# Performance work log

Measured on AMD Instinct MI355X. Metric: run time of the kernel, lower is better.

## Reference

```python
import jax, jax.numpy as jnp
import numpy as np

EPS = 1e-5

def _conv1x1(x, w, b=None):
    # x: (B, Cin, H, W), w: (Cout, Cin) -> (B, Cout, H, W)
    y = jnp.einsum('bchw,oc->bohw', x, w)
    if b is not None:
        y = y + b[None, :, None, None]
    return y

def setup_inputs() -> dict:
    key = jax.random.key(0)
    ks = jax.random.split(key, 14)
    B, C, I = 4, 256, 128
    Ha = Wa = 64
    Hd = Wd = 128
    s = 0.05
    return {
        'detect':  jax.random.normal(ks[0], (B, C, Hd, Wd), jnp.float32),
        'aim':     jax.random.normal(ks[1], (B, C, Ha, Wa), jnp.float32),
        'g_w':     jax.random.normal(ks[2], (I, C), jnp.float32) * s,
        'g_b':     jax.random.normal(ks[3], (I,), jnp.float32) * s,
        'theta_w': jax.random.normal(ks[4], (I, C), jnp.float32) * s,
        'theta_b': jax.random.normal(ks[5], (I,), jnp.float32) * s,
        'phi_w':   jax.random.normal(ks[6], (I, C), jnp.float32) * s,
        'phi_b':   jax.random.normal(ks[7], (I,), jnp.float32) * s,
        'q_w':     jax.random.normal(ks[8], (C, I), jnp.float32) * s,
        'q_b':     jax.random.normal(ks[9], (C,), jnp.float32) * s,
        'bn_gamma': jax.random.normal(ks[10], (C,), jnp.float32),
        'bn_beta':  jax.random.normal(ks[11], (C,), jnp.float32),
        'bn_mean':  jax.random.normal(ks[12], (C,), jnp.float32),
        'bn_var':   jax.random.uniform(ks[13], (C,), jnp.float32) + 0.5,
    }

def reference(detect, aim, g_w, g_b, theta_w, theta_b, phi_w, phi_b,
              q_w, q_b, bn_gamma, bn_beta, bn_mean, bn_var):
    B, C, Hd, Wd = detect.shape
    _, _, Ha, Wa = aim.shape
    Na = Ha * Wa
    Nd = Hd * Wd
    I = g_w.shape[0]

    # 1x1 conv projections, flattened to token sequences
    a_g   = _conv1x1(aim, g_w, g_b).reshape(B, I, Na)        # g(aim)
    th_a  = _conv1x1(aim, theta_w, theta_b).reshape(B, I, Na)
    ph_d  = _conv1x1(detect, phi_w, phi_b).reshape(B, I, Nd)
    # (d_x = g(detect) is dead code in the original forward; omitted)

    # f = theta_x @ phi_x : (B, Na, Nd); permuted -> (B, Nd, Na); N = Na
    f = jnp.einsum('bia,bid->bad', th_a, ph_d)               # (B, Na, Nd)
    inv_n = jnp.float32(1.0 / Na)
    # non_det = (f^T / Na) @ a_x : (B, Nd, I) -> permute -> (B, I, Nd)
    non = jnp.einsum('bad,bia->bid', f * inv_n, a_g)         # (B, I, Nd)
    non = non.reshape(B, I, Hd, Wd)

    # Q: 1x1 conv (I -> C) + BatchNorm (inference mode, running stats)
    y = _conv1x1(non, q_w, q_b)
    inv_std = jax.lax.rsqrt(bn_var + EPS)
    y = (y - bn_mean[None, :, None, None]) * (bn_gamma * inv_std)[None, :, None, None] \
        + bn_beta[None, :, None, None]

    return y + detect
```

## Files before the change

### kernel.cpp

```cpp
#include <hip/hip_runtime.h>

constexpr int BB   = 4;
constexpr int CCH  = 256;
constexpr int IDIM = 128;
constexpr int NAa  = 4096;
constexpr int NDd  = 16384;
constexpr int PAD  = 320;
constexpr float NAinv = 1.0f / 4096.0f;

typedef __bf16 bf16x8 __attribute__((ext_vector_type(8)));
typedef float  f32x4  __attribute__((ext_vector_type(4)));

__device__ inline unsigned short f2bfu(float f) {
    unsigned u = __float_as_uint(f);
    u += 0x7FFFu + ((u >> 16) & 1u);
    return (unsigned short)(u >> 16);
}

__global__ __launch_bounds__(256) void k_conv(const float* __restrict__ aim,
                                              unsigned short* __restrict__ Abf,
                                              float* __restrict__ r) {
    const int row = blockIdx.x;
    const float* src = aim + (long)row * NAa;
    unsigned short* dst = Abf + (long)row * NAa;
    const int t = threadIdx.x;
    float s = 0.f;
    #pragma unroll
    for (int j = 0; j < 4; ++j) {
        const int e = (j * 256 + t) * 4;
        float4 v = *(const float4*)(src + e);
        s += v.x + v.y + v.z + v.w;
        ushort4 o; o.x = f2bfu(v.x); o.y = f2bfu(v.y); o.z = f2bfu(v.z); o.w = f2bfu(v.w);
        *(ushort4*)(dst + e) = o;
    }
    __shared__ float red[256];
    red[t] = s; __syncthreads();
    for (int st = 128; st > 0; st >>= 1) { if (t < st) red[t] += red[t + st]; __syncthreads(); }
    if (t == 0) r[row] = red[0];
}

__global__ __launch_bounds__(256) void k_prep(const float* __restrict__ qw,
                                              const float* __restrict__ gw,
                                              const float* __restrict__ gb,
                                              const float* __restrict__ thw,
                                              const float* __restrict__ thb,
                                              const float* __restrict__ phw,
                                              const float* __restrict__ phb,
                                              unsigned short* __restrict__ Ph,
                                              unsigned short* __restrict__ Rt) {
    const int idx = blockIdx.x * 256 + threadIdx.x;
    if (idx < CCH * PAD) {
        const int o = idx / PAD, c = idx - o * PAD;
        float acc = 0.f;
        if (c <= 256) {
            for (int i = 0; i < IDIM; ++i)
                acc += qw[o * IDIM + i] * ((c < 256) ? gw[i * CCH + c] : gb[i]);
        }
        Ph[idx] = f2bfu(acc);
    } else {
        const int id2 = idx - CCH * PAD;
        const int c2 = id2 / PAD, k = id2 - c2 * PAD;
        float acc = 0.f;
        if (k <= 256 && c2 <= 256) {
            for (int i = 0; i < IDIM; ++i) {
                const float av = (k < 256) ? thw[i * CCH + k] : thb[i];
                const float bv = (c2 < 256) ? phw[i * CCH + c2] : phb[i];
                acc += av * bv;
            }
        }
        Rt[id2] = f2bfu(acc);
    }
}

__global__ __launch_bounds__(64) void k_S(const unsigned short* __restrict__ Abf,
                                          float* __restrict__ Spart) {
    const int z = blockIdx.z, b = z >> 3, chunk = z & 7;
    const unsigned short* A = Abf + (long)b * CCH * NAa;
    const int lane = threadIdx.x, quad = lane >> 4, l16 = lane & 15;
    const int mb = blockIdx.y * 64, nb = blockIdx.x * 64;
    const int kb = chunk * 512;
    f32x4 acc[4][4] = {};
    for (int ks = 0; ks < 16; ++ks) {
        const int k = kb + ks * 32 + quad * 8;
        bf16x8 af[4], bfr[4];
        #pragma unroll
        for (int i = 0; i < 4; ++i) af[i]  = *(const bf16x8*)(A + (long)(mb + i * 16 + l16) * NAa + k);
        #pragma unroll
        for (int j = 0; j < 4; ++j) bfr[j] = *(const bf16x8*)(A + (long)(nb + j * 16 + l16) * NAa + k);
        #pragma unroll
        for (int i = 0; i < 4; ++i)
            #pragma unroll
            for (int j = 0; j < 4; ++j)
                acc[i][j] = __builtin_amdgcn_mfma_f32_16x16x32_bf16(af[i], bfr[j], acc[i][j], 0, 0, 0);
    }
    float* o = Spart + (long)z * CCH * CCH;
    #pragma unroll
    for (int i = 0; i < 4; ++i)
        #pragma unroll
        for (int j = 0; j < 4; ++j)
            #pragma unroll
            for (int reg = 0; reg < 4; ++reg)
                o[(long)(mb + i * 16 + quad * 4 + reg) * CCH + nb + j * 16 + l16] = acc[i][j][reg];
}

__global__ __launch_bounds__(256) void k_red(const float* __restrict__ Spart,
                                             const float* __restrict__ r,
                                             unsigned short* __restrict__ Shat) {
    const int b = blockIdx.y;
    const int idx = blockIdx.x * 256 + threadIdx.x;
    const int k = idx / PAD, n = idx - k * PAD;
    float v = 0.f;
    if (k < 256 && n < 256) {
        #pragma unroll
        for (int p = 0; p < 8; ++p)
            v += Spart[(long)(b * 8 + p) * CCH * CCH + k * CCH + n];
    } else if (k == 256 && n < 256) v = r[b * CCH + n];
    else if (n == 256 && k < 256)   v = r[b * CCH + k];
    else if (k == 256 && n == 256)  v = 4096.0f;
    Shat[(long)b * PAD * PAD + idx] = f2bfu(v);
}

__global__ __launch_bounds__(64) void k_t1(const unsigned short* __restrict__ Ph,
                                           const unsigned short* __restrict__ Sh,
                                           unsigned short* __restrict__ Th) {
    const int b = blockIdx.z;
    const unsigned short* S = Sh + (long)b * PAD * PAD;
    unsigned short* T = Th + (long)b * CCH * PAD;
    const int n0 = blockIdx.x * 64, m0 = blockIdx.y * 64;
    const int lane = threadIdx.x, quad = lane >> 4, l16 = lane & 15;
    f32x4 acc[4][4] = {};
    for (int kt = 0; kt < PAD; kt += 32) {
        bf16x8 af[4], bfr[4];
        #pragma unroll
        for (int i = 0; i < 4; ++i) af[i]  = *(const bf16x8*)(Ph + (long)(m0 + i * 16 + l16) * PAD + kt + quad * 8);
        #pragma unroll
        for (int j = 0; j < 4; ++j) bfr[j] = *(const bf16x8*)(S  + (long)(n0 + j * 16 + l16) * PAD + kt + quad * 8);
        #pragma unroll
        for (int i = 0; i < 4; ++i)
            #pragma unroll
            for (int j = 0; j < 4; ++j)
                acc[i][j] = __builtin_amdgcn_mfma_f32_16x16x32_bf16(af[i], bfr[j], acc[i][j], 0, 0, 0);
    }
    #pragma unroll
    for (int i = 0; i < 4; ++i)
        #pragma unroll
        for (int j = 0; j < 4; ++j)
            #pragma unroll
            for (int reg = 0; reg < 4; ++reg)
                T[(long)(m0 + i * 16 + quad * 4 + reg) * PAD + n0 + j * 16 + l16] = f2bfu(acc[i][j][reg]);
}

__global__ __launch_bounds__(64) void k_t2(const unsigned short* __restrict__ Th,
                                           const unsigned short* __restrict__ Rt,
                                           const float* __restrict__ qb,
                                           const float* __restrict__ gamma,
                                           const float* __restrict__ beta,
                                           const float* __restrict__ mean,
                                           const float* __restrict__ var,
                                           unsigned short* __restrict__ W5u,
                                           float* __restrict__ b5) {
    const int b = blockIdx.z;
    const unsigned short* A = Th + (long)b * CCH * PAD;
    const int n0 = blockIdx.x * 64, m0 = blockIdx.y * 64;
    const int lane = threadIdx.x, quad = lane >> 4, l16 = lane & 15;
    f32x4 acc[4][4] = {};
    for (int kt = 0; kt < PAD; kt += 32) {
        bf16x8 af[4], bfr[4];
        #pragma unroll
        for (int i = 0; i < 4; ++i) af[i]  = *(const bf16x8*)(A  + (long)(m0 + i * 16 + l16) * PAD + kt + quad * 8);
        #pragma unroll
        for (int j = 0; j < 4; ++j) bfr[j] = *(const bf16x8*)(Rt + (long)(n0 + j * 16 + l16) * PAD + kt + quad * 8);
        #pragma unroll
        for (int i = 0; i < 4; ++i)
            #pragma unroll
            for (int j = 0; j < 4; ++j)
                acc[i][j] = __builtin_amdgcn_mfma_f32_16x16x32_bf16(af[i], bfr[j], acc[i][j], 0, 0, 0);
    }
    #pragma unroll
    for (int i = 0; i < 4; ++i) {
        #pragma unroll
        for (int reg = 0; reg < 4; ++reg) {
            const int o = m0 + i * 16 + quad * 4 + reg;
            const float s = gamma[o] * rsqrtf(var[o] + 1e-5f);
            #pragma unroll
            for (int j = 0; j < 4; ++j) {
                const int c2 = n0 + j * 16 + l16;
                const float val = acc[i][j][reg] * s * NAinv;
                if (c2 < CCH)
                    W5u[((long)b * CCH + o) * CCH + c2] = f2bfu(val + (o == c2 ? 1.0f : 0.0f));
                else if (c2 == CCH)
                    b5[b * CCH + o] = val + s * (qb[o] - mean[o]) + beta[o];
            }
        }
    }
}

__global__ __launch_bounds__(256) void k_final(const float* __restrict__ D0,
                                               const unsigned short* __restrict__ W5u,
                                               const float* __restrict__ b5,
                                               float* __restrict__ out) {
    const int z = blockIdx.z;
    const int nb = blockIdx.x * 128;
    const int ob = blockIdx.y * 128;
    const float* D = D0 + (long)z * CCH * NDd;
    float* O = out + (long)z * CCH * NDd;
    const unsigned short* W = W5u + (long)z * CCH * CCH;
    const int t = threadIdx.x, wv = t >> 6, lane = t & 63, quad = lane >> 4, l16 = lane & 15;
    const int mw = (wv >> 1) * 64, nw = (wv & 1) * 64;
    const int r2 = t >> 4, g = t & 15;
    __shared__ __align__(16) unsigned short lb[2][128][40];

    f32x4 xa[4], xb[4];
    bf16x8 af[2][4], bfr[4];

    auto load_tile = [&](f32x4* x, int kt) {
        const float* base = D + (long)(kt + 2 * r2) * NDd + nb + 8 * g;
        x[0] = *(const f32x4*)(base);
        x[1] = *(const f32x4*)(base + NDd);
        x[2] = *(const f32x4*)(base + 4);
        x[3] = *(const f32x4*)(base + NDd + 4);
    };
    auto write_tile = [&](int buf, const f32x4* x) {
        #pragma unroll
        for (int e2 = 0; e2 < 2; ++e2)
            #pragma unroll
            for (int c = 0; c < 4; ++c) {
                const int n = 8 * g + 4 * e2 + c;
                const int p = ((n & 7) << 4) + (n >> 3);
                const unsigned v = (unsigned)f2bfu(x[2 * e2][c]) |
                                   ((unsigned)f2bfu(x[2 * e2 + 1][c]) << 16);
                *(unsigned*)&lb[buf][p][2 * r2] = v;
            }
    };
    auto loadW = [&](bf16x8* a, int kt) {
        #pragma unroll
        for (int i = 0; i < 4; ++i)
            a[i] = *(const bf16x8*)(W + (long)(ob + mw + i * 16 + l16) * CCH + kt + quad * 8);
    };

    int pj[4];
    #pragma unroll
    for (int j = 0; j < 4; ++j) {
        const int n = nw + j * 16 + l16;
        pj[j] = ((n & 7) << 4) + (n >> 3);
    }

    f32x4 acc[4][4] = {};
    load_tile(xa, 0);
    load_tile(xb, 32);
    loadW(af[0], 0);
    write_tile(0, xa);
    load_tile(xa, 64);
    #pragma unroll
    for (int it = 0; it < 8; ++it) {
        __syncthreads();
        const int kt = it * 32;
        #pragma unroll
        for (int j = 0; j < 4; ++j)
            bfr[j] = *(const bf16x8*)&lb[it & 1][pj[j]][quad * 8];
        #pragma unroll
        for (int i = 0; i < 4; ++i)
            #pragma unroll
            for (int j = 0; j < 4; ++j)
                acc[i][j] = __builtin_amdgcn_mfma_f32_16x16x32_bf16(af[it & 1][i], bfr[j], acc[i][j], 0, 0, 0);
        if (it < 7) {
            loadW(af[(it + 1) & 1], kt + 32);
            write_tile((it + 1) & 1, (it & 1) ? xa : xb);
            if (it < 5) load_tile((it & 1) ? xa : xb, (it + 3) * 32);
        }
    }
    #pragma unroll
    for (int i = 0; i < 4; ++i) {
        float bv[4];
        #pragma unroll
        for (int reg = 0; reg < 4; ++reg)
            bv[reg] = b5[z * CCH + ob + mw + i * 16 + quad * 4 + reg];
        #pragma unroll
        for (int j = 0; j < 4; ++j) {
            const int n = nb + nw + j * 16 + l16;
            #pragma unroll
            for (int reg = 0; reg < 4; ++reg)
                O[(long)(ob + mw + i * 16 + quad * 4 + reg) * NDd + n] = acc[i][j][reg] + bv[reg];
        }
    }
}

extern "C" void kernel_launch(void* const* d_in, const int* in_sizes, int n_in,
                              void* d_out, int out_size, void* d_ws, size_t ws_size,
                              hipStream_t stream) {
    const float* detect = (const float*)d_in[0];
    const float* aim    = (const float*)d_in[1];
    const float* g_w    = (const float*)d_in[2];
    const float* g_b    = (const float*)d_in[3];
    const float* th_w   = (const float*)d_in[4];
    const float* th_b   = (const float*)d_in[5];
    const float* phi_w  = (const float*)d_in[6];
    const float* phi_b  = (const float*)d_in[7];
    const float* q_w    = (const float*)d_in[8];
    const float* q_b    = (const float*)d_in[9];
    const float* gamma  = (const float*)d_in[10];
    const float* beta   = (const float*)d_in[11];
    const float* mean   = (const float*)d_in[12];
    const float* var    = (const float*)d_in[13];
    float* out = (float*)d_out;

    float* ws = (float*)d_ws;
    unsigned short* Abf = (unsigned short*)ws;
    float* r     = ws + 2097152;
    float* Spart = r + 1024;
    unsigned short* ub = (unsigned short*)(Spart + 2097152);
    unsigned short* Shat_u  = ub;
    unsigned short* Phat_u  = Shat_u + 409600;
    unsigned short* RhatT_u = Phat_u + 81920;
    unsigned short* That_u  = RhatT_u + 102400;
    unsigned short* W5u     = That_u + 327680;
    float* b5 = (float*)(W5u + 262144);

    k_prep<<<dim3((CCH * PAD + PAD * PAD) / 256), dim3(256), 0, stream>>>(
        q_w, g_w, g_b, th_w, th_b, phi_w, phi_b, Phat_u, RhatT_u);
    k_conv<<<dim3(BB * CCH), dim3(256), 0, stream>>>(aim, Abf, r);
    k_S<<<dim3(4, 4, BB * 8), dim3(64), 0, stream>>>(Abf, Spart);
    k_red<<<dim3(PAD * PAD / 256, BB), dim3(256), 0, stream>>>(Spart, r, Shat_u);
    k_t1<<<dim3(5, 4, BB), dim3(64), 0, stream>>>(Phat_u, Shat_u, That_u);
    k_t2<<<dim3(5, 4, BB), dim3(64), 0, stream>>>(That_u, RhatT_u, q_b, gamma, beta, mean, var, W5u, b5);
    k_final<<<dim3(NDd / 128, CCH / 128, BB), dim3(256), 0, stream>>>(detect, W5u, b5, out);
}
```

Measured before the change: 216.8 us.

## Fuse front kernels, merge T1/T2 via LDS, widen final GEMM to all channels

Merges the aim conversion and weight-prep kernels into one launch, and fuses the two small chained GEMMs (k_t1, k_t2) into a single kernel that keeps the intermediate T tile in shared memory. The final kernel now uses 512 threads per block covering all 256 output channels, so each detect tile is loaded and converted once instead of twice. Only half the threads stage detect into LDS. The fused T kernel launches only 16 blocks, which lowers parallelism in that stage.

```diff
diff --git a/kernel.cpp b/kernel.cpp
--- a/kernel.cpp
+++ b/kernel.cpp
@@ -17,58 +17,59 @@
     return (unsigned short)(u >> 16);
 }
 
-__global__ __launch_bounds__(256) void k_conv(const float* __restrict__ aim,
-                                              unsigned short* __restrict__ Abf,
-                                              float* __restrict__ r) {
-    const int row = blockIdx.x;
-    const float* src = aim + (long)row * NAa;
-    unsigned short* dst = Abf + (long)row * NAa;
+__global__ __launch_bounds__(256) void k_front(const float* __restrict__ aim,
+                                               unsigned short* __restrict__ Abf,
+                                               float* __restrict__ r,
+                                               const float* __restrict__ qw,
+                                               const float* __restrict__ gw,
+                                               const float* __restrict__ gb,
+                                               const float* __restrict__ thw,
+                                               const float* __restrict__ thb,
+                                               const float* __restrict__ phw,
+                                               const float* __restrict__ phb,
+                                               unsigned short* __restrict__ Ph,
+                                               unsigned short* __restrict__ Rt) {
+    __shared__ float red[256];
     const int t = threadIdx.x;
-    float s = 0.f;
-    #pragma unroll
-    for (int j = 0; j < 4; ++j) {
-        const int e = (j * 256 + t) * 4;
-        float4 v = *(const float4*)(src + e);
-        s += v.x + v.y + v.z + v.w;
-        ushort4 o; o.x = f2bfu(v.x); o.y = f2bfu(v.y); o.z = f2bfu(v.z); o.w = f2bfu(v.w);
-        *(ushort4*)(dst + e) = o;
-    }
-    __shared__ float red[256];
-    red[t] = s; __syncthreads();
-    for (int st = 128; st > 0; st >>= 1) { if (t < st) red[t] += red[t + st]; __syncthreads(); }
-    if (t == 0) r[row] = red[0];
-}
-
-__global__ __launch_bounds__(256) void k_prep(const float* __restrict__ qw,
-                                              const float* __restrict__ gw,
-                                              const float* __restrict__ gb,
-                                              const float* __restrict__ thw,
-                                              const float* __restrict__ thb,
-                                              const float* __restrict__ phw,
-                                              const float* __restrict__ phb,
-                                              unsigned short* __restrict__ Ph,
-                                              unsigned short* __restrict__ Rt) {
-    const int idx = blockIdx.x * 256 + threadIdx.x;
-    if (idx < CCH * PAD) {
-        const int o = idx / PAD, c = idx - o * PAD;
-        float acc = 0.f;
-        if (c <= 256) {
-            for (int i = 0; i < IDIM; ++i)
-                acc += qw[o * IDIM + i] * ((c < 256) ? gw[i * CCH + c] : gb[i]);
-        }
-        Ph[idx] = f2bfu(acc);
+    if (blockIdx.x < BB * CCH) {
+        const int row = blockIdx.x;
+        const float* src = aim + (long)row * NAa;
+        unsigned short* dst = Abf + (long)row * NAa;
+        float s = 0.f;
+        #pragma unroll
+        for (int j = 0; j < 4; ++j) {
+            const int e = (j * 256 + t) * 4;
+            float4 v = *(const float4*)(src + e);
+            s += v.x + v.y + v.z + v.w;
+            ushort4 o; o.x = f2bfu(v.x); o.y = f2bfu(v.y); o.z = f2bfu(v.z); o.w = f2bfu(v.w);
+            *(ushort4*)(dst + e) = o;
+        }
+        red[t] = s; __syncthreads();
+        for (int st = 128; st > 0; st >>= 1) { if (t < st) red[t] += red[t + st]; __syncthreads(); }
+        if (t == 0) r[row] = red[0];
     } else {
-        const int id2 = idx - CCH * PAD;
-        const int c2 = id2 / PAD, k = id2 - c2 * PAD;
-        float acc = 0.f;
-        if (k <= 256 && c2 <= 256) {
-            for (int i = 0; i < IDIM; ++i) {
-                const float av = (k < 256) ? thw[i * CCH + k] : thb[i];
-                const float bv = (c2 < 256) ? phw[i * CCH + c2] : phb[i];
-                acc += av * bv;
-            }
-        }
-        Rt[id2] = f2bfu(acc);
+        const int idx = (blockIdx.x - BB * CCH) * 256 + t;
+        if (idx < CCH * PAD) {
+            const int o = idx / PAD, c = idx - o * PAD;
+            float acc = 0.f;
+            if (c <= 256) {
+                for (int i = 0; i < IDIM; ++i)
+                    acc += qw[o * IDIM + i] * ((c < 256) ? gw[i * CCH + c] : gb[i]);
+            }
+            Ph[idx] = f2bfu(acc);
+        } else {
+            const int id2 = idx - CCH * PAD;
+            const int c2 = id2 / PAD, k = id2 - c2 * PAD;
+            float acc = 0.f;
+            if (k <= 256 && c2 <= 256) {
+                for (int i = 0; i < IDIM; ++i) {
+                    const float av = (k < 256) ? thw[i * CCH + k] : thb[i];
+                    const float bv = (c2 < 256) ? phw[i * CCH + c2] : phb[i];
+                    acc += av * bv;
+                }
+            }
+            Rt[id2] = f2bfu(acc);
+        }
     }
 }
 
@@ -120,37 +121,8 @@
     Shat[(long)b * PAD * PAD + idx] = f2bfu(v);
 }
 
-__global__ __launch_bounds__(64) void k_t1(const unsigned short* __restrict__ Ph,
+__global__ __launch_bounds__(256) void k_t(const unsigned short* __restrict__ Ph,
                                            const unsigned short* __restrict__ Sh,
-                                           unsigned short* __restrict__ Th) {
-    const int b = blockIdx.z;
-    const unsigned short* S = Sh + (long)b * PAD * PAD;
-    unsigned short* T = Th + (long)b * CCH * PAD;
-    const int n0 = blockIdx.x * 64, m0 = blockIdx.y * 64;
-    const int lane = threadIdx.x, quad = lane >> 4, l16 = lane & 15;
-    f32x4 acc[4][4] = {};
-    for (int kt = 0; kt < PAD; kt += 32) {
-        bf16x8 af[4], bfr[4];
-        #pragma unroll
-        for (int i = 0; i < 4; ++i) af[i]  = *(const bf16x8*)(Ph + (long)(m0 + i * 16 + l16) * PAD + kt + quad * 8);
-        #pragma unroll
-        for (int j = 0; j < 4; ++j) bfr[j] = *(const bf16x8*)(S  + (long)(n0 + j * 16 + l16) * PAD + kt + quad * 8);
-        #pragma unroll
-        for (int i = 0; i < 4; ++i)
-            #pragma unroll
-            for (int j = 0; j < 4; ++j)
-                acc[i][j] = __builtin_amdgcn_mfma_f32_16x16x32_bf16(af[i], bfr[j], acc[i][j], 0, 0, 0);
-    }
-    #pragma unroll
-    for (int i = 0; i < 4; ++i)
-        #pragma unroll
-        for (int j = 0; j < 4; ++j)
-            #pragma unroll
-            for (int reg = 0; reg < 4; ++reg)
-                T[(long)(m0 + i * 16 + quad * 4 + reg) * PAD + n0 + j * 16 + l16] = f2bfu(acc[i][j][reg]);
-}
-
-__global__ __launch_bounds__(64) void k_t2(const unsigned short* __restrict__ Th,
                                            const unsigned short* __restrict__ Rt,
                                            const float* __restrict__ qb,
                                            const float* __restrict__ gamma,
@@ -159,55 +131,89 @@
                                            const float* __restrict__ var,
                                            unsigned short* __restrict__ W5u,
                                            float* __restrict__ b5) {
-    const int b = blockIdx.z;
-    const unsigned short* A = Th + (long)b * CCH * PAD;
-    const int n0 = blockIdx.x * 64, m0 = blockIdx.y * 64;
-    const int lane = threadIdx.x, quad = lane >> 4, l16 = lane & 15;
-    f32x4 acc[4][4] = {};
-    for (int kt = 0; kt < PAD; kt += 32) {
-        bf16x8 af[4], bfr[4];
-        #pragma unroll
-        for (int i = 0; i < 4; ++i) af[i]  = *(const bf16x8*)(A  + (long)(m0 + i * 16 + l16) * PAD + kt + quad * 8);
-        #pragma unroll
-        for (int j = 0; j < 4; ++j) bfr[j] = *(const bf16x8*)(Rt + (long)(n0 + j * 16 + l16) * PAD + kt + quad * 8);
+    const int b = blockIdx.y;
+    const int m0 = blockIdx.x * 64;
+    const unsigned short* S = Sh + (long)b * PAD * PAD;
+    const int t = threadIdx.x, w = t >> 6, lane = t & 63, quad = lane >> 4, l16 = lane & 15;
+    __shared__ __align__(16) unsigned short Tl[64][328];
+
+    {
+        f32x4 a1[4][5] = {};
+        for (int kt = 0; kt < PAD; kt += 32) {
+            bf16x8 af[4], bfr[5];
+            #pragma unroll
+            for (int i = 0; i < 4; ++i)
+                af[i] = *(const bf16x8*)(Ph + (long)(m0 + i * 16 + l16) * PAD + kt + quad * 8);
+            #pragma unroll
+            for (int j = 0; j < 5; ++j)
+                bfr[j] = *(const bf16x8*)(S + (long)(w * 80 + j * 16 + l16) * PAD + kt + quad * 8);
+            #pragma unroll
+            for (int i = 0; i < 4; ++i)
+                #pragma unroll
+                for (int j = 0; j < 5; ++j)
+                    a1[i][j] = __builtin_amdgcn_mfma_f32_16x16x32_bf16(af[i], bfr[j], a1[i][j], 0, 0, 0);
+        }
         #pragma unroll
         for (int i = 0; i < 4; ++i)
             #pragma unroll
+            for (int j = 0; j < 5; ++j)
+                #pragma unroll
+                for (int reg = 0; reg < 4; ++reg)
+                    Tl[i * 16 + quad * 4 + reg][w * 80 + j * 16 + l16] = f2bfu(a1[i][j][reg]);
+    }
+    __syncthreads();
+
+    for (int pass = 0; pass < 2; ++pass) {
+        if (pass == 1 && w != 0) break;
+        const int n0 = (pass == 0) ? w * 64 : 256;
+        f32x4 acc[4][4] = {};
+        for (int kt = 0; kt < PAD; kt += 32) {
+            bf16x8 af[4], bfr[4];
+            #pragma unroll
+            for (int i = 0; i < 4; ++i)
+                af[i] = *(const bf16x8*)&Tl[i * 16 + l16][kt + quad * 8];
+            #pragma unroll
             for (int j = 0; j < 4; ++j)
-                acc[i][j] = __builtin_amdgcn_mfma_f32_16x16x32_bf16(af[i], bfr[j], acc[i][j], 0, 0, 0);
-    }
-    #pragma unroll
-    for (int i = 0; i < 4; ++i) {
-        #pragma unroll
-        for (int reg = 0; reg < 4; ++reg) {
-            const int o = m0 + i * 16 + quad * 4 + reg;
-            const float s = gamma[o] * rsqrtf(var[o] + 1e-5f);
-            #pragma unroll
-            for (int j = 0; j < 4; ++j) {
-                const int c2 = n0 + j * 16 + l16;
-                const float val = acc[i][j][reg] * s * NAinv;
-                if (c2 < CCH)
-                    W5u[((long)b * CCH + o) * CCH + c2] = f2bfu(val + (o == c2 ? 1.0f : 0.0f));
-                else if (c2 == CCH)
-                    b5[b * CCH + o] = val + s * (qb[o] - mean[o]) + beta[o];
-            }
-        }
-    }
-}
-
-__global__ __launch_bounds__(256) void k_final(const float* __restrict__ D0,
+                bfr[j] = *(const bf16x8*)(Rt + (long)(n0 + j * 16 + l16) * PAD + kt + quad * 8);
+            #pragma unroll
+            for (int i = 0; i < 4; ++i)
+                #pragma unroll
+                for (int j = 0; j < 4; ++j)
+                    acc[i][j] = __builtin_amdgcn_mfma_f32_16x16x32_bf16(af[i], bfr[j], acc[i][j], 0, 0, 0);
+        }
+        #pragma unroll
+        for (int i = 0; i < 4; ++i) {
+            #pragma unroll
+            for (int reg = 0; reg < 4; ++reg) {
+                const int o = m0 + i * 16 + quad * 4 + reg;
+                const float s = gamma[o] * rsqrtf(var[o] + 1e-5f);
+                #pragma unroll
+                for (int j = 0; j < 4; ++j) {
+                    const int c2 = n0 + j * 16 + l16;
+                    const float val = acc[i][j][reg] * s * NAinv;
+                    if (c2 < CCH)
+                        W5u[((long)b * CCH + o) * CCH + c2] = f2bfu(val + (o == c2 ? 1.0f : 0.0f));
+                    else if (c2 == CCH)
+                        b5[b * CCH + o] = val + s * (qb[o] - mean[o]) + beta[o];
+                }
+            }
+        }
+    }
+}
+
+__global__ __launch_bounds__(512) void k_final(const float* __restrict__ D0,
                                                const unsigned short* __restrict__ W5u,
                                                const float* __restrict__ b5,
                                                float* __restrict__ out) {
     const int z = blockIdx.z;
     const int nb = blockIdx.x * 128;
-    const int ob = blockIdx.y * 128;
     const float* D = D0 + (long)z * CCH * NDd;
     float* O = out + (long)z * CCH * NDd;
     const unsigned short* W = W5u + (long)z * CCH * CCH;
     const int t = threadIdx.x, wv = t >> 6, lane = t & 63, quad = lane >> 4, l16 = lane & 15;
     const int mw = (wv >> 1) * 64, nw = (wv & 1) * 64;
     const int r2 = t >> 4, g = t & 15;
+    const bool st = (t < 256);
     __shared__ __align__(16) unsigned short lb[2][128][40];
 
     f32x4 xa[4], xb[4];
@@ -235,7 +241,7 @@
     auto loadW = [&](bf16x8* a, int kt) {
         #pragma unroll
         for (int i = 0; i < 4; ++i)
-            a[i] = *(const bf16x8*)(W + (long)(ob + mw + i * 16 + l16) * CCH + kt + quad * 8);
+            a[i] = *(const bf16x8*)(W + (long)(mw + i * 16 + l16) * CCH + kt + quad * 8);
     };
 
     int pj[4];
@@ -246,11 +252,9 @@
     }
 
     f32x4 acc[4][4] = {};
-    load_tile(xa, 0);
-    load_tile(xb, 32);
+    if (st) { load_tile(xa, 0); load_tile(xb, 32); }
     loadW(af[0], 0);
-    write_tile(0, xa);
-    load_tile(xa, 64);
+    if (st) { write_tile(0, xa); load_tile(xa, 64); }
     #pragma unroll
     for (int it = 0; it < 8; ++it) {
         __syncthreads();
@@ -265,8 +269,10 @@
                 acc[i][j] = __builtin_amdgcn_mfma_f32_16x16x32_bf16(af[it & 1][i], bfr[j], acc[i][j], 0, 0, 0);
         if (it < 7) {
             loadW(af[(it + 1) & 1], kt + 32);
-            write_tile((it + 1) & 1, (it & 1) ? xa : xb);
-            if (it < 5) load_tile((it & 1) ? xa : xb, (it + 3) * 32);
+            if (st) {
+                write_tile((it + 1) & 1, (it & 1) ? xa : xb);
+                if (it < 5) load_tile((it & 1) ? xa : xb, (it + 3) * 32);
+            }
         }
     }
     #pragma unroll
@@ -274,13 +280,13 @@
         float bv[4];
         #pragma unroll
         for (int reg = 0; reg < 4; ++reg)
-            bv[reg] = b5[z * CCH + ob + mw + i * 16 + quad * 4 + reg];
+            bv[reg] = b5[z * CCH + mw + i * 16 + quad * 4 + reg];
         #pragma unroll
         for (int j = 0; j < 4; ++j) {
             const int n = nb + nw + j * 16 + l16;
             #pragma unroll
             for (int reg = 0; reg < 4; ++reg)
-                O[(long)(ob + mw + i * 16 + quad * 4 + reg) * NDd + n] = acc[i][j][reg] + bv[reg];
+                O[(long)(mw + i * 16 + quad * 4 + reg) * NDd + n] = acc[i][j][reg] + bv[reg];
         }
     }
 }
@@ -316,12 +322,10 @@
     unsigned short* W5u     = That_u + 327680;
     float* b5 = (float*)(W5u + 262144);
 
-    k_prep<<<dim3((CCH * PAD + PAD * PAD) / 256), dim3(256), 0, stream>>>(
-        q_w, g_w, g_b, th_w, th_b, phi_w, phi_b, Phat_u, RhatT_u);
-    k_conv<<<dim3(BB * CCH), dim3(256), 0, stream>>>(aim, Abf, r);
+    k_front<<<dim3(BB * CCH + (CCH * PAD + PAD * PAD) / 256), dim3(256), 0, stream>>>(
+        aim, Abf, r, q_w, g_w, g_b, th_w, th_b, phi_w, phi_b, Phat_u, RhatT_u);
     k_S<<<dim3(4, 4, BB * 8), dim3(64), 0, stream>>>(Abf, Spart);
     k_red<<<dim3(PAD * PAD / 256, BB), dim3(256), 0, stream>>>(Spart, r, Shat_u);
-    k_t1<<<dim3(5, 4, BB), dim3(64), 0, stream>>>(Phat_u, Shat_u, That_u);
-    k_t2<<<dim3(5, 4, BB), dim3(64), 0, stream>>>(That_u, RhatT_u, q_b, gamma, beta, mean, var, W5u, b5);
-    k_final<<<dim3(NDd / 128, CCH / 128, BB), dim3(256), 0, stream>>>(detect, W5u, b5, out);
-}
+    k_t<<<dim3(4, BB), dim3(256), 0, stream>>>(Phat_u, Shat_u, RhatT_u, q_b, gamma, beta, mean, var, W5u, b5);
+    k_final<<<dim3(NDd / 128, 1, BB), dim3(512), 0, stream>>>(detect, W5u, b5, out);
+}
```

Result: slower. 228.7 us (+5.5%).
